# Performance work log

Measured on AMD Instinct MI355X. Metric: run time of the kernel, lower is better.

Reference implementation:

```python
import jax, jax.numpy as jnp
import numpy as np
import math

D_MODEL = 1024
N_HEADS = 16
D_HID = 64
B, L = 2, 2048
NEG = -1e9
EPS = 1e-5


def setup_inputs() -> dict:
    key = jax.random.key(0)
    ks = jax.random.split(key, 16)
    dmh = N_HEADS * D_HID
    s_in = 1.0 / math.sqrt(D_MODEL)
    s_out = 1.0 / math.sqrt(dmh)
    return {
        "Q": jax.random.normal(ks[0], (B, L, D_MODEL), jnp.float32),
        "K": jax.random.normal(ks[1], (B, L, D_MODEL), jnp.float32),
        "V": jax.random.normal(ks[2], (B, L, D_MODEL), jnp.float32),
        "atten_mask": jax.random.randint(ks[3], (B, L, L), 0, 2) > 0,
        "Wq": jax.random.normal(ks[4], (D_MODEL, dmh), jnp.float32) * s_in,
        "bq": jnp.zeros((dmh,), jnp.float32),
        "Wk": jax.random.normal(ks[5], (D_MODEL, dmh), jnp.float32) * s_in,
        "bk": jnp.zeros((dmh,), jnp.float32),
        "Wv": jax.random.normal(ks[6], (D_MODEL, dmh), jnp.float32) * s_in,
        "bv": jnp.zeros((dmh,), jnp.float32),
        "Wo": jax.random.normal(ks[7], (dmh, D_MODEL), jnp.float32) * s_out,
        "bo": jnp.zeros((D_MODEL,), jnp.float32),
        "gamma": jnp.ones((D_MODEL,), jnp.float32),
        "beta": jnp.zeros((D_MODEL,), jnp.float32),
    }


def reference(Q, K, V, atten_mask, Wq, bq, Wk, bk, Wv, bv, Wo, bo, gamma, beta):
    b = Q.shape[0]
    # project and split heads: [B, L, H, Dh] -> [B, H, L, Dh]
    q = (Q @ Wq + bq).reshape(b, -1, N_HEADS, D_HID).transpose(0, 2, 1, 3)
    k = (K @ Wk + bk).reshape(b, -1, N_HEADS, D_HID).transpose(0, 2, 1, 3)
    v = (V @ Wv + bv).reshape(b, -1, N_HEADS, D_HID).transpose(0, 2, 1, 3)
    scale = 1.0 / math.sqrt(D_HID)
    scores = jnp.einsum("bhqd,bhkd->bhqk", q, k * scale)
    scores = jnp.where(atten_mask[:, None, :, :], NEG, scores)
    atten = jax.nn.softmax(scores, axis=-1)
    context = jnp.einsum("bhqk,bhkd->bhqd", atten, v)
    context = context.transpose(0, 2, 1, 3).reshape(b, -1, N_HEADS * D_HID)
    out = context @ Wo + bo
    # residual + LayerNorm
    x = out + Q
    mu = jnp.mean(x, axis=-1, keepdims=True)
    var = jnp.var(x, axis=-1, keepdims=True)
    y = (x - mu) * jax.lax.rsqrt(var + EPS) * gamma + beta
    return (y, atten)
```

## Files before the change

### kernel.cpp

```cpp
#include <hip/hip_runtime.h>
#include <hip/hip_fp16.h>

typedef unsigned short u16;
typedef __attribute__((ext_vector_type(8))) _Float16 f16x8;
typedef __attribute__((ext_vector_type(2))) _Float16 f16x2;
typedef __attribute__((ext_vector_type(4))) float   f32x4;

typedef const __attribute__((address_space(1))) void* gas1_t;
typedef __attribute__((address_space(3))) void*       las3_t;

#define LOG2E 1.44269504089f
#define M12   17.3123404907f

__device__ __forceinline__ void async_ld16(const void* g, void* s){
  __builtin_amdgcn_global_load_lds((gas1_t)g, (las3_t)s, 16, 0, 0);
}
__device__ __forceinline__ u16 f2h(float f){
  return __half_as_ushort(__float2half(f));
}

__global__ void cvt3_kernel(const float* __restrict__ s0, const float* __restrict__ s1,
                            const float* __restrict__ s2, u16* __restrict__ d0,
                            u16* __restrict__ d1, u16* __restrict__ d2)
{
  const float* s = (blockIdx.y==0)? s0 : (blockIdx.y==1)? s1 : s2;
  u16* d = (blockIdx.y==0)? d0 : (blockIdx.y==1)? d1 : d2;
  for(int i = blockIdx.x*256 + threadIdx.x; i < 1048576; i += 512*256){
    float4 v = ((const float4*)s)[i];
    ushort4 o; o.x=f2h(v.x); o.y=f2h(v.y); o.z=f2h(v.z); o.w=f2h(v.w);
    ((ushort4*)d)[i] = o;
  }
}

__global__ void transcvt_kernel(const float* __restrict__ W0, const float* __restrict__ W1,
                                const float* __restrict__ W2, const float* __restrict__ W3,
                                u16* __restrict__ T0, u16* __restrict__ T1,
                                u16* __restrict__ T2, u16* __restrict__ T3)
{
  __shared__ float tile[64][65];
  int z = blockIdx.z;
  const float* W = (z==0)?W0:(z==1)?W1:(z==2)?W2:W3;
  u16* T = (z==0)?T0:(z==1)?T1:(z==2)?T2:T3;
  int k0 = blockIdx.y*64, n0v = blockIdx.x*64;
  int t = threadIdx.x, r = t>>4, c4 = (t&15)*4;
#pragma unroll
  for(int p=0;p<4;p++){
    int rr = p*16 + r;
    float4 v = *(const float4*)&W[(size_t)(k0+rr)*1024 + n0v + c4];
    tile[rr][c4+0]=v.x; tile[rr][c4+1]=v.y; tile[rr][c4+2]=v.z; tile[rr][c4+3]=v.w;
  }
  __syncthreads();
#pragma unroll
  for(int p=0;p<4;p++){
    int rr = p*16 + r;
    ushort4 o;
    o.x = f2h(tile[c4+0][rr]); o.y = f2h(tile[c4+1][rr]);
    o.z = f2h(tile[c4+2][rr]); o.w = f2h(tile[c4+3][rr]);
    *(ushort4*)&T[(size_t)(n0v+rr)*1024 + k0 + c4] = o;
  }
}

__global__ void mask_detect_kernel(const unsigned int* __restrict__ m, int* __restrict__ flag){
  __shared__ int any;
  if(threadIdx.x==0) any = 0;
  __syncthreads();
  int bad = 0;
  for(int i=threadIdx.x;i<2048;i+=256) if(m[i] > 1u) bad = 1;
  if(bad) any = 1;
  __syncthreads();
  if(threadIdx.x==0) *flag = any;
}

__global__ void mask_bits_kernel(const void* __restrict__ msrc, const int* __restrict__ flag,
                                 unsigned long long* __restrict__ mbits)
{
  int gw = (blockIdx.x*256 + threadIdx.x)>>6;
  int lane = threadIdx.x & 63;
  int f = *flag;
  for(int c=0;c<32;c++){
    int idx = gw*2048 + c*64 + lane;
    unsigned v = f ? (unsigned)((const unsigned char*)msrc)[idx]
                   : ((const unsigned int*)msrc)[idx];
    unsigned long long bal = __ballot(v != 0u);
    if(lane==0) mbits[gw*32 + c] = bal;
  }
}

__device__ __forceinline__ void gemm_kloop(const u16* __restrict__ A, const u16* __restrict__ BT,
                                           int m0, int n0, u16* lA, u16* lB, f32x4 acc[4][4])
{
  int t = threadIdx.x, w = t>>6, l = t&63, l4 = l>>4, lm = l&15;
  int wr = w>>1, wc = w&1;
  for(int k0=0;k0<1024;k0+=32){
#pragma unroll
    for(int j=0;j<2;j++){
      int idx = j*4096 + w*1024 + l*16;
      int r = idx>>6, cb = idx&63;
      int cbs = cb ^ ((r&3)<<4);
      async_ld16((const char*)A  + (((size_t)(m0+r))<<11) + k0*2 + cbs,
                 (char*)lA + j*4096 + w*1024);
      async_ld16((const char*)BT + (((size_t)(n0+r))<<11) + k0*2 + cbs,
                 (char*)lB + j*4096 + w*1024);
    }
    __syncthreads();
    f16x8 af[4], bfr[4];
#pragma unroll
    for(int m=0;m<4;m++){
      int ar = wr*64 + m*16 + lm;
      af[m] = *(const f16x8*)((const char*)lA + ar*64 + ((l4*16) ^ ((ar&3)<<4)));
    }
#pragma unroll
    for(int n=0;n<4;n++){
      int br = wc*64 + n*16 + lm;
      bfr[n] = *(const f16x8*)((const char*)lB + br*64 + ((l4*16) ^ ((br&3)<<4)));
    }
#pragma unroll
    for(int m=0;m<4;m++)
#pragma unroll
      for(int n=0;n<4;n++)
        acc[m][n] = __builtin_amdgcn_mfma_f32_16x16x32_f16(af[m], bfr[n], acc[m][n], 0,0,0);
    __syncthreads();
  }
}

__global__ __launch_bounds__(256) void proj_gemm(
    const u16* __restrict__ Xq, const u16* __restrict__ Xk, const u16* __restrict__ Xv,
    const u16* __restrict__ WqT, const u16* __restrict__ WkT, const u16* __restrict__ WvT,
    const float* __restrict__ bq, const float* __restrict__ bk, const float* __restrict__ bv,
    u16* __restrict__ qb, u16* __restrict__ kbuf, u16* __restrict__ vTb)
{
  __shared__ u16 lA[4096], lB[4096];
  int z = blockIdx.z;
  const u16* A  = (z==0)?Xq :(z==1)?Xk :Xv;
  const u16* BT = (z==0)?WqT:(z==1)?WkT:WvT;
  const float* bias = (z==0)?bq:(z==1)?bk:bv;
  int m0 = blockIdx.y*128, n0 = blockIdx.x*128;
  f32x4 zf = {0.f,0.f,0.f,0.f};
  f32x4 acc[4][4];
#pragma unroll
  for(int m=0;m<4;m++)
#pragma unroll
    for(int n=0;n<4;n++) acc[m][n]=zf;
  gemm_kloop(A, BT, m0, n0, lA, lB, acc);

  int t = threadIdx.x, w = t>>6, l = t&63, l4 = l>>4, lm = l&15;
  int wr = w>>1, wc = w&1;
  float scale = (z==1)? 0.125f : 1.0f;
#pragma unroll
  for(int n=0;n<4;n++){
    int ng = n0 + wc*64 + n*16 + lm;
    float bsv = bias[ng];
#pragma unroll
    for(int m=0;m<4;m++){
      int mb = m0 + wr*64 + m*16 + l4*4;
      f32x4 c = acc[m][n];
      int bhh = ((mb>>11)<<4) + (ng>>6);
      if(z<2){
        u16* dst = (z==0)? qb : kbuf;
        size_t base = (((size_t)bhh)<<17) + ((size_t)(mb&2047)<<6) + (ng&63);
        dst[base      ] = f2h((c[0]+bsv)*scale);
        dst[base +  64] = f2h((c[1]+bsv)*scale);
        dst[base + 128] = f2h((c[2]+bsv)*scale);
        dst[base + 192] = f2h((c[3]+bsv)*scale);
      } else {
        size_t off = (((size_t)bhh)<<17) + ((size_t)(ng&63)<<11) + (mb&2047);
        ushort4 o;
        o.x=f2h(c[0]+bsv); o.y=f2h(c[1]+bsv); o.z=f2h(c[2]+bsv); o.w=f2h(c[3]+bsv);
        *(ushort4*)(vTb + off) = o;
      }
    }
  }
}

__global__ __launch_bounds__(256) void attn_fused(
    const u16* __restrict__ qb, const u16* __restrict__ kb,
    const u16* __restrict__ vTb, const unsigned long long* __restrict__ mbits,
    float* __restrict__ att, u16* __restrict__ ctx)
{
  __shared__ u16 ktile[4096];
  __shared__ u16 vtile[4096];
  __shared__ u16 pl[4][16*136];
  int fid = blockIdx.x;
  int xcd = fid & 7, pos = fid >> 3;
  int bh = (xcd<<2) + (pos>>5);
  int q0 = (pos & 31)*64;
  int b = bh>>4, h = bh&15;
  int t = threadIdx.x, w = t>>6, l = t&63, l4 = l>>4, lm = l&15;
  int qw = q0 + w*16 + lm;

  const u16* qrow = qb + ((size_t)bh*2048 + qw)*64;
  f16x8 qB0 = *(const f16x8*)(qrow + l4*8);
  f16x8 qB1 = *(const f16x8*)(qrow + 32 + l4*8);

  const unsigned long long* mrow = mbits + (size_t)(b*2048 + qw)*32;
  const char* kbase_b = (const char*)(kb  + ((size_t)bh<<17));
  const char* vbase_b = (const char*)(vTb + ((size_t)bh<<17));
  f32x4 zf = {0.f,0.f,0.f,0.f};

  float esum = 0.f;
  for(int kt=0;kt<32;kt++){
    int gk = kt*64;
#pragma unroll
    for(int j=0;j<2;j++){
      int idx = j*4096 + t*16, row = idx>>7, cb = idx&127;
      async_ld16(kbase_b + (size_t)(gk+row)*128 + (cb ^ ((row&7)<<4)),
                 (char*)ktile + idx);
    }
    __syncthreads();
    unsigned long long mw = mrow[kt];
    unsigned mlo = (unsigned)mw, mhi = (unsigned)(mw>>32);
#pragma unroll
    for(int kf=0;kf<4;kf++){
      int keyr = kf*16 + lm, sw = (keyr&7)<<4;
      const char* kp = (const char*)ktile + keyr*128;
      f16x8 a0 = *(const f16x8*)(kp + ((l4*16) ^ sw));
      f16x8 a1 = *(const f16x8*)(kp + ((64 + l4*16) ^ sw));
      f32x4 s = __builtin_amdgcn_mfma_f32_16x16x32_f16(a0, qB0, zf, 0,0,0);
      s = __builtin_amdgcn_mfma_f32_16x16x32_f16(a1, qB1, s, 0,0,0);
      unsigned nib = (((kf&2)?mhi:mlo) >> ((kf&1)*16 + l4*4)) & 15u;
      esum += exp2f(((nib&1u)? -1e9f : s[0])*LOG2E - M12);
      esum += exp2f(((nib&2u)? -1e9f : s[1])*LOG2E - M12);
      esum += exp2f(((nib&4u)? -1e9f : s[2])*LOG2E - M12);
      esum += exp2f(((nib&8u)? -1e9f : s[3])*LOG2E - M12);
    }
    __syncthreads();
  }
  esum += __shfl_xor(esum, 16);
  esum += __shfl_xor(esum, 32);
  float lrs = -M12 - log2f(fmaxf(esum, 1e-30f));

  f32x4 cacc[4] = {zf,zf,zf,zf};
  int q_hi = l>>5, koff = (l&31)*4;
  float* abase = att + ((size_t)bh*2048 + q0 + w*16)*2048;
  u16* plw = &pl[w][0];

  for(int kg=0; kg<16; kg++){
#pragma unroll
    for(int km=0; km<2; km++){
      int kt = kg*2 + km, gk = kt*64;
#pragma unroll
      for(int j=0;j<2;j++){
        int idx = j*4096 + t*16, row = idx>>7, cb = idx&127;
        async_ld16(kbase_b + (size_t)(gk+row)*128 + (cb ^ ((row&7)<<4)),
                   (char*)ktile + idx);
        async_ld16(vbase_b + (size_t)row*4096 + gk*2 + (cb ^ ((row&7)<<4)),
                   (char*)vtile + idx);
      }
      __syncthreads();
      unsigned long long mw = mrow[kt];
      unsigned mlo = (unsigned)mw, mhi = (unsigned)(mw>>32);
#pragma unroll
      for(int kf=0;kf<4;kf++){
        int keyr = kf*16 + lm, sw = (keyr&7)<<4;
        const char* kp = (const char*)ktile + keyr*128;
        f16x8 a0 = *(const f16x8*)(kp + ((l4*16) ^ sw));
        f16x8 a1 = *(const f16x8*)(kp + ((64 + l4*16) ^ sw));
        f32x4 s = __builtin_amdgcn_mfma_f32_16x16x32_f16(a0, qB0, zf, 0,0,0);
        s = __builtin_amdgcn_mfma_f32_16x16x32_f16(a1, qB1, s, 0,0,0);
        unsigned nib = (((kf&2)?mhi:mlo) >> ((kf&1)*16 + l4*4)) & 15u;
        float p0 = exp2f(((nib&1u)? -1e9f : s[0])*LOG2E + lrs);
        float p1 = exp2f(((nib&2u)? -1e9f : s[1])*LOG2E + lrs);
        float p2 = exp2f(((nib&4u)? -1e9f : s[2])*LOG2E + lrs);
        float p3 = exp2f(((nib&8u)? -1e9f : s[3])*LOG2E + lrs);
        uint2 pk;
        pk.x = __builtin_bit_cast(unsigned, __builtin_amdgcn_cvt_pkrtz(p0,p1));
        pk.y = __builtin_bit_cast(unsigned, __builtin_amdgcn_cvt_pkrtz(p2,p3));
        *(uint2*)(plw + lm*136 + km*64 + kf*16 + l4*4) = pk;
      }
#pragma unroll
      for(int kk=0;kk<2;kk++){
        f16x8 pb = *(const f16x8*)(plw + lm*136 + km*64 + kk*32 + l4*8);
#pragma unroll
        for(int mf=0;mf<4;mf++){
          int dr = mf*16 + lm;
          const char* vp = (const char*)vtile + dr*128;
          f16x8 av = *(const f16x8*)(vp + ((kk*64 + l4*16) ^ ((dr&7)<<4)));
          cacc[mf] = __builtin_amdgcn_mfma_f32_16x16x32_f16(av, pb, cacc[mf], 0,0,0);
        }
      }
      __syncthreads();
    }
#pragma unroll
    for(int qq=0; qq<16; qq+=2){
      int q = qq + q_hi;
      uint2 ph = *(const uint2*)(plw + q*136 + koff);
      f16x2 h0 = __builtin_bit_cast(f16x2, ph.x);
      f16x2 h1 = __builtin_bit_cast(f16x2, ph.y);
      f32x4 o4 = { (float)h0[0], (float)h0[1], (float)h1[0], (float)h1[1] };
      __builtin_nontemporal_store(o4,
          (f32x4*)(abase + (size_t)q*2048 + kg*128 + koff));
    }
  }
  int token = b*2048 + qw;
#pragma unroll
  for(int mf=0;mf<4;mf++){
    ushort4 o;
    o.x=f2h(cacc[mf][0]); o.y=f2h(cacc[mf][1]);
    o.z=f2h(cacc[mf][2]); o.w=f2h(cacc[mf][3]);
    *(ushort4*)(ctx + (size_t)token*1024 + h*64 + mf*16 + l4*4) = o;
  }
}

__global__ __launch_bounds__(256) void out_gemm(
    const u16* __restrict__ ctx, const u16* __restrict__ WoT,
    const float* __restrict__ bo, const float* __restrict__ Qres, float* __restrict__ xout)
{
  __shared__ u16 lA[4096], lB[4096];
  int m0 = blockIdx.y*128, n0 = blockIdx.x*128;
  f32x4 zf = {0.f,0.f,0.f,0.f};
  f32x4 acc[4][4];
#pragma unroll
  for(int m=0;m<4;m++)
#pragma unroll
    for(int n=0;n<4;n++) acc[m][n]=zf;
  gemm_kloop(ctx, WoT, m0, n0, lA, lB, acc);

  int t = threadIdx.x, w = t>>6, l = t&63, l4 = l>>4, lm = l&15;
  int wr = w>>1, wc = w&1;
#pragma unroll
  for(int n=0;n<4;n++){
    int ng = n0 + wc*64 + n*16 + lm;
    float bsv = bo[ng];
#pragma unroll
    for(int m=0;m<4;m++){
      int mb = m0 + wr*64 + m*16 + l4*4;
      f32x4 c = acc[m][n];
#pragma unroll
      for(int j=0;j<4;j++){
        size_t o = ((size_t)(mb+j)<<10) + ng;
        xout[o] = c[j] + bsv + Qres[o];
      }
    }
  }
}

__global__ void ln_kernel(const float* __restrict__ x, const float* __restrict__ gamma,
                          const float* __restrict__ beta, float* __restrict__ y)
{
  int row = blockIdx.x, t = threadIdx.x;
  float4 v = ((const float4*)(x + (size_t)row*1024))[t];
  float s  = v.x+v.y+v.z+v.w;
  float sq = v.x*v.x + v.y*v.y + v.z*v.z + v.w*v.w;
#pragma unroll
  for(int d=1; d<64; d<<=1){ s += __shfl_xor(s, d); sq += __shfl_xor(sq, d); }
  __shared__ float red[8];
  int w = t>>6, l = t&63;
  if(l==0){ red[w] = s; red[4+w] = sq; }
  __syncthreads();
  s  = red[0]+red[1]+red[2]+red[3];
  sq = red[4]+red[5]+red[6]+red[7];
  float mu  = s * 0.0009765625f;
  float var = sq * 0.0009765625f - mu*mu;
  float rs  = rsqrtf(var + 1e-5f);
  float4 g  = ((const float4*)gamma)[t];
  float4 be = ((const float4*)beta)[t];
  float4 o;
  o.x = (v.x-mu)*rs*g.x + be.x;
  o.y = (v.y-mu)*rs*g.y + be.y;
  o.z = (v.z-mu)*rs*g.z + be.z;
  o.w = (v.w-mu)*rs*g.w + be.w;
  ((float4*)(y + (size_t)row*1024))[t] = o;
}

extern "C" void kernel_launch(void* const* d_in, const int* in_sizes, int n_in,
                              void* d_out, int out_size, void* d_ws, size_t ws_size,
                              hipStream_t stream)
{
  (void)in_sizes; (void)n_in; (void)out_size; (void)ws_size;
  const float* Q    = (const float*)d_in[0];
  const float* K    = (const float*)d_in[1];
  const float* V    = (const float*)d_in[2];
  const void*  mraw = d_in[3];
  const float* Wq   = (const float*)d_in[4];
  const float* bq   = (const float*)d_in[5];
  const float* Wk   = (const float*)d_in[6];
  const float* bk   = (const float*)d_in[7];
  const float* Wv   = (const float*)d_in[8];
  const float* bv   = (const float*)d_in[9];
  const float* Wo   = (const float*)d_in[10];
  const float* bo   = (const float*)d_in[11];
  const float* gamma= (const float*)d_in[12];
  const float* beta = (const float*)d_in[13];

  char* ws = (char*)d_ws;
  const size_t MB = 1ull<<20;
  u16* WqT  = (u16*)(ws + 0*MB);
  u16* WkT  = (u16*)(ws + 2*MB);
  u16* WvT  = (u16*)(ws + 4*MB);
  u16* WoT  = (u16*)(ws + 6*MB);
  u16* Xq   = (u16*)(ws + 8*MB);
  u16* Xk   = (u16*)(ws + 16*MB);
  u16* Xv   = (u16*)(ws + 24*MB);
  u16* qb   = (u16*)(ws + 32*MB);
  u16* kbuf = (u16*)(ws + 40*MB);
  u16* vTb  = (u16*)(ws + 48*MB);
  u16* ctx  = (u16*)(ws + 56*MB);
  unsigned long long* mbits = (unsigned long long*)(ws + 8*MB);
  int* flag = (int*)(ws + 10*MB);
  float* xres = (float*)(ws + 16*MB);

  float* yout = (float*)d_out;
  float* att  = (float*)d_out + 4194304;

  cvt3_kernel<<<dim3(512,3,1), 256, 0, stream>>>(Q,K,V,Xq,Xk,Xv);
  transcvt_kernel<<<dim3(16,16,4), 256, 0, stream>>>(Wq,Wk,Wv,Wo,WqT,WkT,WvT,WoT);
  proj_gemm<<<dim3(8,32,3), 256, 0, stream>>>(Xq,Xk,Xv,WqT,WkT,WvT,bq,bk,bv,qb,kbuf,vTb);
  mask_detect_kernel<<<1,256,0,stream>>>((const unsigned int*)mraw, flag);
  mask_bits_kernel<<<1024,256,0,stream>>>(mraw, flag, mbits);
  attn_fused<<<1024, 256, 0, stream>>>(qb,kbuf,vTb,mbits,att,ctx);
  out_gemm<<<dim3(8,32), 256, 0, stream>>>(ctx,WoT,bo,Q,xres);
  ln_kernel<<<4096, 256, 0, stream>>>(xres,gamma,beta,yout);
}
```

Before: 268.5 us.

## Split attention key dimension across wave pairs with 512-thread blocks

Doubles the attention block to 8 waves. Each pair of waves shares a 16-query group and splits every 64-key tile into two 32-key halves, so each wave does half the QK, exp and PV work. Row sums and partial context accumulators are combined through shared memory, and the attention-probability write-out of the previous tile is deferred by one step using a double-buffered P tile. The aim is more waves in flight per CU to hide latency, at the cost of extra barriers, shared-memory reductions and higher LDS pressure.

```diff
diff --git a/kernel.cpp b/kernel.cpp
--- a/kernel.cpp
+++ b/kernel.cpp
@@ -172,52 +172,50 @@
   }
 }
 
-__global__ __launch_bounds__(256) void attn_fused(
+__global__ __launch_bounds__(512, 8) void attn_fused(
     const u16* __restrict__ qb, const u16* __restrict__ kb,
-    const u16* __restrict__ vTb, const unsigned long long* __restrict__ mbits,
+    const u16* __restrict__ vTb, const unsigned* __restrict__ mbits32,
     float* __restrict__ att, u16* __restrict__ ctx)
 {
   __shared__ u16 ktile[4096];
   __shared__ u16 vtile[4096];
-  __shared__ u16 pl[4][16*136];
+  __shared__ u16 pl[4][2][16][72];
+  __shared__ float rsum[4][2][16];
   int fid = blockIdx.x;
   int xcd = fid & 7, pos = fid >> 3;
   int bh = (xcd<<2) + (pos>>5);
   int q0 = (pos & 31)*64;
   int b = bh>>4, h = bh&15;
   int t = threadIdx.x, w = t>>6, l = t&63, l4 = l>>4, lm = l&15;
-  int qw = q0 + w*16 + lm;
+  int qg = w>>1, kh = w&1;
+  int qw = q0 + qg*16 + lm;
 
   const u16* qrow = qb + ((size_t)bh*2048 + qw)*64;
   f16x8 qB0 = *(const f16x8*)(qrow + l4*8);
   f16x8 qB1 = *(const f16x8*)(qrow + 32 + l4*8);
 
-  const unsigned long long* mrow = mbits + (size_t)(b*2048 + qw)*32;
+  const unsigned* mrow = mbits32 + (size_t)(b*2048 + qw)*64 + kh;
   const char* kbase_b = (const char*)(kb  + ((size_t)bh<<17));
   const char* vbase_b = (const char*)(vTb + ((size_t)bh<<17));
   f32x4 zf = {0.f,0.f,0.f,0.f};
 
+  int srow = t>>3, scb = (t&7)*16;
+
   float esum = 0.f;
   for(int kt=0;kt<32;kt++){
-    int gk = kt*64;
-#pragma unroll
-    for(int j=0;j<2;j++){
-      int idx = j*4096 + t*16, row = idx>>7, cb = idx&127;
-      async_ld16(kbase_b + (size_t)(gk+row)*128 + (cb ^ ((row&7)<<4)),
-                 (char*)ktile + idx);
-    }
-    __syncthreads();
-    unsigned long long mw = mrow[kt];
-    unsigned mlo = (unsigned)mw, mhi = (unsigned)(mw>>32);
-#pragma unroll
-    for(int kf=0;kf<4;kf++){
-      int keyr = kf*16 + lm, sw = (keyr&7)<<4;
+    async_ld16(kbase_b + (size_t)(kt*64+srow)*128 + (scb ^ ((srow&7)<<4)),
+               (char*)ktile + t*16);
+    __syncthreads();
+    unsigned mw = mrow[kt*2];
+#pragma unroll
+    for(int kf=0;kf<2;kf++){
+      int keyr = kh*32 + kf*16 + lm, sw = (keyr&7)<<4;
       const char* kp = (const char*)ktile + keyr*128;
       f16x8 a0 = *(const f16x8*)(kp + ((l4*16) ^ sw));
       f16x8 a1 = *(const f16x8*)(kp + ((64 + l4*16) ^ sw));
       f32x4 s = __builtin_amdgcn_mfma_f32_16x16x32_f16(a0, qB0, zf, 0,0,0);
       s = __builtin_amdgcn_mfma_f32_16x16x32_f16(a1, qB1, s, 0,0,0);
-      unsigned nib = (((kf&2)?mhi:mlo) >> ((kf&1)*16 + l4*4)) & 15u;
+      unsigned nib = (mw >> (kf*16 + l4*4)) & 15u;
       esum += exp2f(((nib&1u)? -1e9f : s[0])*LOG2E - M12);
       esum += exp2f(((nib&2u)? -1e9f : s[1])*LOG2E - M12);
       esum += exp2f(((nib&4u)? -1e9f : s[2])*LOG2E - M12);
@@ -227,77 +225,96 @@
   }
   esum += __shfl_xor(esum, 16);
   esum += __shfl_xor(esum, 32);
-  float lrs = -M12 - log2f(fmaxf(esum, 1e-30f));
+  if(l < 16) rsum[qg][kh][l] = esum;
+  __syncthreads();
+  float S = rsum[qg][0][lm] + rsum[qg][1][lm];
+  float lrs = -M12 - log2f(fmaxf(S, 1e-30f));
 
   f32x4 cacc[4] = {zf,zf,zf,zf};
-  int q_hi = l>>5, koff = (l&31)*4;
-  float* abase = att + ((size_t)bh*2048 + q0 + w*16)*2048;
-  u16* plw = &pl[w][0];
-
-  for(int kg=0; kg<16; kg++){
-#pragma unroll
-    for(int km=0; km<2; km++){
-      int kt = kg*2 + km, gk = kt*64;
-#pragma unroll
-      for(int j=0;j<2;j++){
-        int idx = j*4096 + t*16, row = idx>>7, cb = idx&127;
-        async_ld16(kbase_b + (size_t)(gk+row)*128 + (cb ^ ((row&7)<<4)),
-                   (char*)ktile + idx);
-        async_ld16(vbase_b + (size_t)row*4096 + gk*2 + (cb ^ ((row&7)<<4)),
-                   (char*)vtile + idx);
+  float* abase = att + ((size_t)bh*2048 + q0 + qg*16)*2048;
+
+  for(int kt=0; kt<32; kt++){
+    async_ld16(kbase_b + (size_t)(kt*64+srow)*128 + (scb ^ ((srow&7)<<4)),
+               (char*)ktile + t*16);
+    async_ld16(vbase_b + (size_t)srow*4096 + kt*128 + (scb ^ ((srow&7)<<4)),
+               (char*)vtile + t*16);
+    __syncthreads();
+    unsigned mw = mrow[kt*2];
+    u16* plc = &pl[qg][kt&1][0][0];
+#pragma unroll
+    for(int kf=0;kf<2;kf++){
+      int keyr = kh*32 + kf*16 + lm, sw = (keyr&7)<<4;
+      const char* kp = (const char*)ktile + keyr*128;
+      f16x8 a0 = *(const f16x8*)(kp + ((l4*16) ^ sw));
+      f16x8 a1 = *(const f16x8*)(kp + ((64 + l4*16) ^ sw));
+      f32x4 s = __builtin_amdgcn_mfma_f32_16x16x32_f16(a0, qB0, zf, 0,0,0);
+      s = __builtin_amdgcn_mfma_f32_16x16x32_f16(a1, qB1, s, 0,0,0);
+      unsigned nib = (mw >> (kf*16 + l4*4)) & 15u;
+      float p0 = exp2f(((nib&1u)? -1e9f : s[0])*LOG2E + lrs);
+      float p1 = exp2f(((nib&2u)? -1e9f : s[1])*LOG2E + lrs);
+      float p2 = exp2f(((nib&4u)? -1e9f : s[2])*LOG2E + lrs);
+      float p3 = exp2f(((nib&8u)? -1e9f : s[3])*LOG2E + lrs);
+      uint2 pk;
+      pk.x = __builtin_bit_cast(unsigned, __builtin_amdgcn_cvt_pkrtz(p0,p1));
+      pk.y = __builtin_bit_cast(unsigned, __builtin_amdgcn_cvt_pkrtz(p2,p3));
+      *(uint2*)(plc + lm*72 + kh*32 + kf*16 + l4*4) = pk;
+    }
+    f16x8 pb = *(const f16x8*)(plc + lm*72 + kh*32 + l4*8);
+#pragma unroll
+    for(int mf=0;mf<4;mf++){
+      int dr = mf*16 + lm;
+      f16x8 av = *(const f16x8*)((const char*)vtile + dr*128 +
+                                 ((kh*64 + l4*16) ^ ((dr&7)<<4)));
+      cacc[mf] = __builtin_amdgcn_mfma_f32_16x16x32_f16(av, pb, cacc[mf], 0,0,0);
+    }
+    __syncthreads();
+    if(kt > 0){
+      int tp = kt-1;
+      const u16* src = &pl[qg][tp&1][0][0];
+#pragma unroll
+      for(int s2=0;s2<2;s2++){
+        int fi = kh*512 + s2*256 + l*4;
+        int r = fi>>6, c = fi&63;
+        uint2 ph = *(const uint2*)(src + r*72 + c);
+        f16x2 h0 = __builtin_bit_cast(f16x2, ph.x);
+        f16x2 h1 = __builtin_bit_cast(f16x2, ph.y);
+        f32x4 o4 = { (float)h0[0], (float)h0[1], (float)h1[0], (float)h1[1] };
+        __builtin_nontemporal_store(o4,
+            (f32x4*)(abase + (size_t)r*2048 + tp*64 + c));
       }
-      __syncthreads();
-      unsigned long long mw = mrow[kt];
-      unsigned mlo = (unsigned)mw, mhi = (unsigned)(mw>>32);
-#pragma unroll
-      for(int kf=0;kf<4;kf++){
-        int keyr = kf*16 + lm, sw = (keyr&7)<<4;
-        const char* kp = (const char*)ktile + keyr*128;
-        f16x8 a0 = *(const f16x8*)(kp + ((l4*16) ^ sw));
-        f16x8 a1 = *(const f16x8*)(kp + ((64 + l4*16) ^ sw));
-        f32x4 s = __builtin_amdgcn_mfma_f32_16x16x32_f16(a0, qB0, zf, 0,0,0);
-        s = __builtin_amdgcn_mfma_f32_16x16x32_f16(a1, qB1, s, 0,0,0);
-        unsigned nib = (((kf&2)?mhi:mlo) >> ((kf&1)*16 + l4*4)) & 15u;
-        float p0 = exp2f(((nib&1u)? -1e9f : s[0])*LOG2E + lrs);
-        float p1 = exp2f(((nib&2u)? -1e9f : s[1])*LOG2E + lrs);
-        float p2 = exp2f(((nib&4u)? -1e9f : s[2])*LOG2E + lrs);
-        float p3 = exp2f(((nib&8u)? -1e9f : s[3])*LOG2E + lrs);
-        uint2 pk;
-        pk.x = __builtin_bit_cast(unsigned, __builtin_amdgcn_cvt_pkrtz(p0,p1));
-        pk.y = __builtin_bit_cast(unsigned, __builtin_amdgcn_cvt_pkrtz(p2,p3));
-        *(uint2*)(plw + lm*136 + km*64 + kf*16 + l4*4) = pk;
-      }
-#pragma unroll
-      for(int kk=0;kk<2;kk++){
-        f16x8 pb = *(const f16x8*)(plw + lm*136 + km*64 + kk*32 + l4*8);
-#pragma unroll
-        for(int mf=0;mf<4;mf++){
-          int dr = mf*16 + lm;
-          const char* vp = (const char*)vtile + dr*128;
-          f16x8 av = *(const f16x8*)(vp + ((kk*64 + l4*16) ^ ((dr&7)<<4)));
-          cacc[mf] = __builtin_amdgcn_mfma_f32_16x16x32_f16(av, pb, cacc[mf], 0,0,0);
-        }
-      }
-      __syncthreads();
-    }
-#pragma unroll
-    for(int qq=0; qq<16; qq+=2){
-      int q = qq + q_hi;
-      uint2 ph = *(const uint2*)(plw + q*136 + koff);
+    }
+  }
+  {
+    const u16* src = &pl[qg][31&1][0][0];
+#pragma unroll
+    for(int s2=0;s2<2;s2++){
+      int fi = kh*512 + s2*256 + l*4;
+      int r = fi>>6, c = fi&63;
+      uint2 ph = *(const uint2*)(src + r*72 + c);
       f16x2 h0 = __builtin_bit_cast(f16x2, ph.x);
       f16x2 h1 = __builtin_bit_cast(f16x2, ph.y);
       f32x4 o4 = { (float)h0[0], (float)h0[1], (float)h1[0], (float)h1[1] };
       __builtin_nontemporal_store(o4,
-          (f32x4*)(abase + (size_t)q*2048 + kg*128 + koff));
-    }
-  }
-  int token = b*2048 + qw;
-#pragma unroll
-  for(int mf=0;mf<4;mf++){
-    ushort4 o;
-    o.x=f2h(cacc[mf][0]); o.y=f2h(cacc[mf][1]);
-    o.z=f2h(cacc[mf][2]); o.w=f2h(cacc[mf][3]);
-    *(ushort4*)(ctx + (size_t)token*1024 + h*64 + mf*16 + l4*4) = o;
+          (f32x4*)(abase + (size_t)r*2048 + 31*64 + c));
+    }
+  }
+
+  __syncthreads();
+  float* sc = (qg<2)? (float*)ktile + qg*1024 : (float*)vtile + (qg-2)*1024;
+  if(kh==1){
+#pragma unroll
+    for(int mf=0;mf<4;mf++) *(f32x4*)(sc + mf*256 + l*4) = cacc[mf];
+  }
+  __syncthreads();
+  if(kh==0){
+    int token = b*2048 + qw;
+#pragma unroll
+    for(int mf=0;mf<4;mf++){
+      f32x4 o = cacc[mf] + *(const f32x4*)(sc + mf*256 + l*4);
+      ushort4 u;
+      u.x=f2h(o[0]); u.y=f2h(o[1]); u.z=f2h(o[2]); u.w=f2h(o[3]);
+      *(ushort4*)(ctx + (size_t)token*1024 + h*64 + mf*16 + l4*4) = u;
+    }
   }
 }
 
@@ -407,7 +424,7 @@
   proj_gemm<<<dim3(8,32,3), 256, 0, stream>>>(Xq,Xk,Xv,WqT,WkT,WvT,bq,bk,bv,qb,kbuf,vTb);
   mask_detect_kernel<<<1,256,0,stream>>>((const unsigned int*)mraw, flag);
   mask_bits_kernel<<<1024,256,0,stream>>>(mraw, flag, mbits);
-  attn_fused<<<1024, 256, 0, stream>>>(qb,kbuf,vTb,mbits,att,ctx);
+  attn_fused<<<1024, 512, 0, stream>>>(qb,kbuf,vTb,(const unsigned*)mbits,att,ctx);
   out_gemm<<<dim3(8,32), 256, 0, stream>>>(ctx,WoT,bo,Q,xres);
   ln_kernel<<<4096, 256, 0, stream>>>(xres,gamma,beta,yout);
 }
```

After: 264.5 us. About the same (-1.5%).
